# Performance work log

Hardware: AMD Instinct MI355X
Metric: run time of the kernel (lower is better)

## Reference

```python
import jax, jax.numpy as jnp
import numpy as np

S, B, H, NH = 2048, 2, 1024, 16
DH = H // NH

def setup_inputs() -> dict:
    key = jax.random.key(0)
    ks = jax.random.split(key, 4)
    x = jax.random.normal(ks[0], (S, B, H), dtype=jnp.float32)
    attention_mask = jnp.ones((B, 1, S, S), dtype=bool)
    rotary_pos_emb = jax.random.uniform(ks[1], (S, 1, 1, DH), dtype=jnp.float32)
    Wqkv = jax.random.normal(ks[2], (H, 3 * H), dtype=jnp.float32) * (1.0 / np.sqrt(H))
    bqkv = jnp.zeros((3 * H,), dtype=jnp.float32)
    Wproj = jax.random.normal(ks[3], (H, H), dtype=jnp.float32) * (1.0 / np.sqrt(H))
    bproj = jnp.zeros((H,), dtype=jnp.float32)
    return {"x": x, "attention_mask": attention_mask, "rotary_pos_emb": rotary_pos_emb,
            "Wqkv": Wqkv, "bqkv": bqkv, "Wproj": Wproj, "bproj": bproj}

def reference(x, attention_mask, rotary_pos_emb, Wqkv, bqkv, Wproj, bproj):
    s, b, h = x.shape
    dh = h // NH
    # QKV projection; per-head layout [s,b,NH,3*dh] then split (matches view+chunk)
    qkv = (x @ Wqkv + bqkv).reshape(s, b, NH, 3 * dh)
    q, k, v = jnp.split(qkv, 3, axis=-1)  # each [s,b,NH,dh]
    # RoPE (non-interleaved, rot_dim == head_dim)
    cos = jnp.cos(rotary_pos_emb)  # [s,1,1,dh]
    sin = jnp.sin(rotary_pos_emb)
    def rope(t):
        t1, t2 = jnp.split(t, 2, axis=-1)
        return t * cos + jnp.concatenate((-t2, t1), axis=-1) * sin
    q = rope(q)
    k = rope(k)
    scale = 1.0 / np.sqrt(dh).astype(np.float32)
    # scores: [b,NH,t,s]
    scores = jnp.einsum('tbhd,sbhd->bhts', q, k) * scale
    scores = jnp.where(attention_mask, scores, jnp.float32(-1e9))
    attn = jax.nn.softmax(scores, axis=-1)
    out = jnp.einsum('bhts,sbhd->tbhd', attn, v).reshape(s, b, h)
    return out @ Wproj + bproj
```

## Files before the change

kernel.cpp:

```cpp
#include <hip/hip_runtime.h>
#include <hip/hip_bf16.h>

typedef __attribute__((ext_vector_type(8))) short bf16x8;
typedef __attribute__((ext_vector_type(4))) float f32x4;
typedef __attribute__((ext_vector_type(16))) float f32x16;
typedef __attribute__((ext_vector_type(4))) unsigned short u16x4;

#define S_LEN 2048
#define BATCH 2
#define NHEAD 16
#define DHEAD 64
#define HD    1024
#define MROWS 4096
#define NQKV  3072
#define NBH   32
#define KSPLIT 2
#define KSEG  (S_LEN / KSPLIT)

static __device__ __forceinline__ unsigned short f2bf(float f) {
  union { float f; unsigned u; } v; v.f = f;
  unsigned r = v.u + 0x7FFFu + ((v.u >> 16) & 1u);
  return (unsigned short)(r >> 16);
}
static __device__ __forceinline__ float bf2f(unsigned short h) {
  union { unsigned u; float f; } v; v.u = ((unsigned)h) << 16;
  return v.f;
}
static __device__ __forceinline__ unsigned cvt_pk(float a, float b) {
  unsigned r;
  asm("v_cvt_pk_bf16_f32 %0, %1, %2" : "=v"(r) : "v"(a), "v"(b));
  return r;
}
static __device__ __forceinline__ float exp2_hw(float x) {
  float r;
  asm("v_exp_f32 %0, %1" : "=v"(r) : "v"(x));
  return r;
}

static __device__ __forceinline__ void gl_lds16(const void* g, void* l) {
  __builtin_amdgcn_global_load_lds(
      (__attribute__((address_space(1))) void*)g,
      (__attribute__((address_space(3))) void*)l, 16, 0, 0);
}

__global__ void k_cvt(const float* __restrict__ in, unsigned short* __restrict__ out, int n4) {
  int idx = blockIdx.x * blockDim.x + threadIdx.x;
  int stride = gridDim.x * blockDim.x;
  for (int i = idx; i < n4; i += stride) {
    float4 v = reinterpret_cast<const float4*>(in)[i];
    u16x4 o;
    o.x = f2bf(v.x); o.y = f2bf(v.y); o.z = f2bf(v.z); o.w = f2bf(v.w);
    reinterpret_cast<u16x4*>(out)[i] = o;
  }
}

__global__ void k_transw(const float* __restrict__ W, unsigned short* __restrict__ Wt,
                         int K, int N) {
  __shared__ unsigned short tile[64][72];
  int n0 = blockIdx.x * 64, k0 = blockIdx.y * 64;
  int t = threadIdx.x;
  int r  = t >> 2;
  int c4 = (t & 3) * 16;
  const float* src = W + (size_t)(k0 + r) * N + n0 + c4;
#pragma unroll
  for (int j = 0; j < 16; j += 4) {
    float4 v = *reinterpret_cast<const float4*>(src + j);
    tile[r][c4 + j + 0] = f2bf(v.x);
    tile[r][c4 + j + 1] = f2bf(v.y);
    tile[r][c4 + j + 2] = f2bf(v.z);
    tile[r][c4 + j + 3] = f2bf(v.w);
  }
  __syncthreads();
  int rn = t >> 2;
  int kc = (t & 3) * 16;
  unsigned short* dst = Wt + (size_t)(n0 + rn) * K + k0 + kc;
#pragma unroll
  for (int j = 0; j < 16; j += 8) {
    bf16x8 o;
#pragma unroll
    for (int e = 0; e < 8; ++e) o[e] = (short)tile[kc + j + e][rn];
    *reinterpret_cast<bf16x8*>(dst + j) = o;
  }
}

template <int OUT_BF16, int BN>
__global__ void __launch_bounds__(256)
k_gemm(const unsigned short* __restrict__ A, const unsigned short* __restrict__ Bt,
       const float* __restrict__ bias, void* __restrict__ Cout, int M, int N, int K) {
  constexpr int NF = BN / 32;
  __shared__ unsigned short As[128 * 32];
  __shared__ unsigned short Bs[BN * 32];
  int t = threadIdx.x;
  int lane = t & 63;
  int w = t >> 6;
  int g = lane >> 4, i = lane & 15;
  int wr = w >> 1, wc = w & 1;
  int bx = blockIdx.x, by = blockIdx.y;

  f32x4 acc[4][NF] = {};

  int rowS = ((t >> 6) << 4) + (t & 15);
  int colS = ((t >> 4) & 3) * 8;
  const unsigned short* a_s0 = A  + (size_t)(by * 128 + rowS) * K + colS;
  const unsigned short* a_s1 = A  + (size_t)(by * 128 + 64 + rowS) * K + colS;
  const unsigned short* b_s0 = Bt + (size_t)(bx * BN + rowS) * K + colS;
  const unsigned short* b_s1 = Bt + (size_t)(bx * BN + 64 + rowS) * K + colS;
  unsigned short* a_d0 = &As[t * 8];
  unsigned short* a_d1 = &As[(256 + t) * 8];
  unsigned short* b_d0 = &Bs[t * 8];
  unsigned short* b_d1 = &Bs[(256 + t) * 8];

  for (int kt = 0; kt < K; kt += 32) {
    __syncthreads();
    gl_lds16(a_s0 + kt, a_d0);
    gl_lds16(a_s1 + kt, a_d1);
    gl_lds16(b_s0 + kt, b_d0);
    if constexpr (BN == 128) gl_lds16(b_s1 + kt, b_d1);
    __syncthreads();

    bf16x8 af[4], bf[NF];
#pragma unroll
    for (int m = 0; m < 4; ++m)
      af[m] = *reinterpret_cast<const bf16x8*>(&As[(wr * 256 + m * 64 + lane) * 8]);
#pragma unroll
    for (int n = 0; n < NF; ++n)
      bf[n] = *reinterpret_cast<const bf16x8*>(&Bs[((wc * NF + n) * 64 + lane) * 8]);
#pragma unroll
    for (int m = 0; m < 4; ++m)
#pragma unroll
      for (int n = 0; n < NF; ++n)
        acc[m][n] = __builtin_amdgcn_mfma_f32_16x16x32_bf16(af[m], bf[n], acc[m][n], 0, 0, 0);
  }

  int crow0 = by * 128 + wr * 64;
  int ccol0 = bx * BN + wc * (BN / 2);
#pragma unroll
  for (int n = 0; n < NF; ++n) {
    int col = ccol0 + n * 16 + i;
    float bv = bias[col];
#pragma unroll
    for (int m = 0; m < 4; ++m) {
#pragma unroll
      for (int r = 0; r < 4; ++r) {
        int row = crow0 + m * 16 + g * 4 + r;
        float v = acc[m][n][r] + bv;
        if (OUT_BF16)
          reinterpret_cast<unsigned short*>(Cout)[(size_t)row * N + col] = f2bf(v);
        else
          reinterpret_cast<float*>(Cout)[(size_t)row * N + col] = v;
      }
    }
  }
}

__global__ void k_rope(const unsigned short* __restrict__ QKV, const float* __restrict__ rot,
                       unsigned short* __restrict__ Qg, unsigned short* __restrict__ Kg,
                       unsigned short* __restrict__ Vg) {
  __shared__ unsigned short vtile[32][72];
  int s0 = blockIdx.x * 32;
  int bh = blockIdx.y;
  int b = bh >> 4, nh = bh & 15;
  int t = threadIdx.x;
  int c  = t & 31;
  int hi = (t >> 5) & 1;
  int ks = t >> 6;
  int d0 = ks * 16 + hi * 8;
  int s = s0 + c;
  const unsigned short* base = QKV + ((size_t)s * BATCH + b) * NQKV + nh * 192;

  float cs[8], sn[8];
#pragma unroll
  for (int j = 0; j < 8; j += 4) {
    float4 rv = *reinterpret_cast<const float4*>(rot + (size_t)s * DHEAD + d0 + j);
    cs[j + 0] = cosf(rv.x); sn[j + 0] = sinf(rv.x);
    cs[j + 1] = cosf(rv.y); sn[j + 1] = sinf(rv.y);
    cs[j + 2] = cosf(rv.z); sn[j + 2] = sinf(rv.z);
    cs[j + 3] = cosf(rv.w); sn[j + 3] = sinf(rv.w);
  }
  float sgn = (d0 < 32) ? -1.f : 1.f;
  bf16x8 qv = *reinterpret_cast<const bf16x8*>(base + d0);
  bf16x8 qp = *reinterpret_cast<const bf16x8*>(base + (d0 ^ 32));
  bf16x8 kv = *reinterpret_cast<const bf16x8*>(base + 64 + d0);
  bf16x8 kp = *reinterpret_cast<const bf16x8*>(base + 64 + (d0 ^ 32));
  bf16x8 qo, ko;
#pragma unroll
  for (int j = 0; j < 8; ++j) {
    float q = bf2f((unsigned short)qv[j]) * cs[j] + sgn * bf2f((unsigned short)qp[j]) * sn[j];
    float k = bf2f((unsigned short)kv[j]) * cs[j] + sgn * bf2f((unsigned short)kp[j]) * sn[j];
    qo[j] = (short)f2bf(q * 0.18033688f);
    ko[j] = (short)f2bf(k);
  }
  size_t blk = ((size_t)bh * (S_LEN / 32) + (s0 >> 5)) * 2048;
  *reinterpret_cast<bf16x8*>(Qg + blk + t * 8) = qo;
  *reinterpret_cast<bf16x8*>(Kg + blk + t * 8) = ko;

  bf16x8 vv = *reinterpret_cast<const bf16x8*>(base + 128 + d0);
  *reinterpret_cast<bf16x8*>(&vtile[c][d0]) = vv;
  __syncthreads();
  int vbr = t >> 7, h = (t >> 6) & 1, hi2 = (t >> 5) & 1, cc = t & 31;
  int d = 32 * h + cc;
  bf16x8 vo;
#pragma unroll
  for (int j = 0; j < 8; ++j) vo[j] = (short)vtile[vbr * 16 + hi2 * 8 + j][d];
  size_t vblk = ((size_t)bh * (S_LEN / 16) + (s0 >> 4) + vbr) * 1024;
  *reinterpret_cast<bf16x8*>(Vg + vblk + (t & 127) * 8) = vo;
}


static __device__ __forceinline__ void sm_pv(const f32x16& sc, const bf16x8* vfr,
                                             float& l_acc, f32x16& o0, f32x16& o1) {
  float p[16];
#pragma unroll
  for (int r = 0; r < 16; ++r) p[r] = exp2_hw(sc[r]);
  float s0 = (p[0] + p[1]) + (p[2] + p[3]);
  float s1 = (p[4] + p[5]) + (p[6] + p[7]);
  float s2 = (p[8] + p[9]) + (p[10] + p[11]);
  float s3 = (p[12] + p[13]) + (p[14] + p[15]);
  l_acc += (s0 + s1) + (s2 + s3);
#pragma unroll
  for (int ksl = 0; ksl < 2; ++ksl) {
    unsigned A0 = cvt_pk(p[8 * ksl + 0], p[8 * ksl + 1]);
    unsigned A1 = cvt_pk(p[8 * ksl + 2], p[8 * ksl + 3]);
    unsigned A2 = cvt_pk(p[8 * ksl + 4], p[8 * ksl + 5]);
    unsigned A3 = cvt_pk(p[8 * ksl + 6], p[8 * ksl + 7]);
    asm volatile("v_permlane32_swap_b32 %0, %1" : "+v"(A0), "+v"(A2));
    asm volatile("v_permlane32_swap_b32 %0, %1" : "+v"(A1), "+v"(A3));
    union { unsigned u[4]; bf16x8 v; } pa;
    pa.u[0] = A0; pa.u[1] = A1; pa.u[2] = A2; pa.u[3] = A3;
    __builtin_amdgcn_s_setprio(1);
    o0 = __builtin_amdgcn_mfma_f32_32x32x16_bf16(pa.v, vfr[2 * ksl + 0], o0, 0, 0, 0);
    o1 = __builtin_amdgcn_mfma_f32_32x32x16_bf16(pa.v, vfr[2 * ksl + 1], o1, 0, 0, 0);
    __builtin_amdgcn_s_setprio(0);
  }
}

__global__ void __launch_bounds__(256, 2)
k_flash(const unsigned short* __restrict__ Qg, const unsigned short* __restrict__ Kg,
        const unsigned short* __restrict__ Vg, unsigned short* __restrict__ Opart,
        float* __restrict__ Lpart) {
  __shared__ unsigned short kv_lds[2 * 8192];
  int bh = blockIdx.x, qt = blockIdx.y, kv = blockIdx.z;
  int t = threadIdx.x, lane = t & 63;
  int c = lane & 31, hi = lane >> 5;

  int q0 = qt * 128 + (t >> 6) * 32;
  int kv0 = kv * KSEG;
  const unsigned short* Qb = Qg + (size_t)bh * S_LEN * DHEAD + (size_t)q0 * DHEAD;
  const unsigned short* Kb = Kg + (size_t)bh * S_LEN * DHEAD;
  const unsigned short* Vb = Vg + (size_t)bh * S_LEN * DHEAD;

  bf16x8 qf[4];
#pragma unroll
  for (int ks = 0; ks < 4; ++ks)
    qf[ks] = *reinterpret_cast<const bf16x8*>(Qb + ((size_t)ks * 64 + lane) * 8);

#define STAGE(kt, bufi) do {                                                   \
    const unsigned short* _ks = Kb + (size_t)(kt) * DHEAD;                     \
    const unsigned short* _vs = Vb + (size_t)(kt) * DHEAD;                     \
    unsigned short* _kd = &kv_lds[(bufi) * 8192];                              \
    unsigned short* _vd = _kd + 4096;                                          \
    gl_lds16(_ks + t * 8, _kd + t * 8);                                        \
    gl_lds16(_ks + (t + 256) * 8, _kd + (t + 256) * 8);                        \
    gl_lds16(_vs + t * 8, _vd + t * 8);                                        \
    gl_lds16(_vs + (t + 256) * 8, _vd + (t + 256) * 8);                        \
  } while (0)

  f32x16 o0 = {}, o1 = {};
  float l_acc = 0.f;
  int cur = 0;

  STAGE(kv0, 0);
  for (int kt = kv0; kt < kv0 + KSEG; kt += 64) {
    __syncthreads();
    int nxt = kv0 + (((kt - kv0) + 64) & (KSEG - 1));
    STAGE(nxt, cur ^ 1);

    const unsigned short* kbuf = &kv_lds[cur * 8192];
    const unsigned short* vbuf = kbuf + 4096;

    f32x16 scA = {}, scB = {};
    __builtin_amdgcn_s_setprio(1);
#pragma unroll
    for (int ks = 0; ks < 4; ++ks) {
      bf16x8 kf = *reinterpret_cast<const bf16x8*>(kbuf + (ks * 64 + lane) * 8);
      scA = __builtin_amdgcn_mfma_f32_32x32x16_bf16(kf, qf[ks], scA, 0, 0, 0);
    }
#pragma unroll
    for (int ks = 0; ks < 4; ++ks) {
      bf16x8 kf = *reinterpret_cast<const bf16x8*>(kbuf + (256 + ks * 64 + lane) * 8);
      scB = __builtin_amdgcn_mfma_f32_32x32x16_bf16(kf, qf[ks], scB, 0, 0, 0);
    }
    __builtin_amdgcn_s_setprio(0);

    bf16x8 va[4], vb[4];
#pragma unroll
    for (int g = 0; g < 2; ++g) {
      va[2 * g + 0] = *reinterpret_cast<const bf16x8*>(vbuf + (g * 128 + lane) * 8);
      va[2 * g + 1] = *reinterpret_cast<const bf16x8*>(vbuf + (g * 128 + 64 + lane) * 8);
      vb[2 * g + 0] = *reinterpret_cast<const bf16x8*>(vbuf + ((g + 2) * 128 + lane) * 8);
      vb[2 * g + 1] = *reinterpret_cast<const bf16x8*>(vbuf + ((g + 2) * 128 + 64 + lane) * 8);
    }

    sm_pv(scA, va, l_acc, o0, o1);
    sm_pv(scB, vb, l_acc, o0, o1);
    cur ^= 1;
  }
#undef STAGE

  float l_tot = l_acc + __shfl_xor(l_acc, 32, 64);

  unsigned short* Op = Opart + ((size_t)kv * NBH + bh) * S_LEN * DHEAD;
  if (hi == 0) Lpart[((size_t)kv * NBH + bh) * S_LEN + q0 + c] = l_tot;
#pragma unroll
  for (int r = 0; r < 16; ++r) {
    int crow = (r & 3) + 8 * (r >> 2) + 4 * hi;
    size_t rowoff = (size_t)(q0 + crow) * DHEAD;
    Op[rowoff + c]      = f2bf(o0[r]);
    Op[rowoff + 32 + c] = f2bf(o1[r]);
  }
}

__global__ void k_reduce(const unsigned short* __restrict__ Op, const float* __restrict__ Lp,
                         unsigned short* __restrict__ attn) {
  const int kvO = NBH * S_LEN * DHEAD;
  const int kvL = NBH * S_LEN;
  int idx = blockIdx.x * blockDim.x + threadIdx.x;
  int row = idx >> 3;
  int d0 = (idx & 7) * 8;
  bf16x8 a = *reinterpret_cast<const bf16x8*>(Op + (size_t)row * DHEAD + d0);
  bf16x8 bq = *reinterpret_cast<const bf16x8*>(Op + kvO + (size_t)row * DHEAD + d0);
  float inv = 1.0f / (Lp[row] + Lp[kvL + row]);
  int bh = row >> 11, q = row & (S_LEN - 1);
  int b = bh >> 4, nh = bh & 15;
  bf16x8 o;
#pragma unroll
  for (int j = 0; j < 8; ++j)
    o[j] = (short)f2bf((bf2f((unsigned short)a[j]) + bf2f((unsigned short)bq[j])) * inv);
  unsigned short* dst = attn + ((size_t)q * BATCH + b) * HD + nh * DHEAD + d0;
  *reinterpret_cast<bf16x8*>(dst) = o;
}

extern "C" void kernel_launch(void* const* d_in, const int* in_sizes, int n_in,
                              void* d_out, int out_size, void* d_ws, size_t ws_size,
                              hipStream_t stream) {
  const float* x     = (const float*)d_in[0];
  const float* rot   = (const float*)d_in[2];
  const float* Wqkv  = (const float*)d_in[3];
  const float* bqkv  = (const float*)d_in[4];
  const float* Wproj = (const float*)d_in[5];
  const float* bproj = (const float*)d_in[6];
  float* out = (float*)d_out;

  char* ws = (char*)d_ws;
  unsigned short* xb   = (unsigned short*)(ws);
  unsigned short* Wqt  = (unsigned short*)(ws + 8388608);
  unsigned short* Wpt  = (unsigned short*)(ws + 14680064);
  unsigned short* QKV  = (unsigned short*)(ws + 16777216);
  unsigned short* Qs   = (unsigned short*)(ws + 41943040);
  unsigned short* Kst  = (unsigned short*)(ws + 50331648);
  unsigned short* Vtt  = (unsigned short*)(ws + 58720256);
  unsigned short* Opart = (unsigned short*)(ws + 16777216);
  float*          Lpart = (float*)(ws + 33554432);
  unsigned short* attn  = xb;

  k_cvt<<<2048, 256, 0, stream>>>(x, xb, MROWS * HD / 4);
  k_transw<<<dim3(NQKV / 64, HD / 64), 256, 0, stream>>>(Wqkv, Wqt, HD, NQKV);
  k_transw<<<dim3(HD / 64, HD / 64), 256, 0, stream>>>(Wproj, Wpt, HD, HD);
  k_gemm<1, 128><<<dim3(NQKV / 128, MROWS / 128), 256, 0, stream>>>(xb, Wqt, bqkv, QKV,
                                                                    MROWS, NQKV, HD);
  k_rope<<<dim3(S_LEN / 32, BATCH * NHEAD), 256, 0, stream>>>(QKV, rot, Qs, Kst, Vtt);
  k_flash<<<dim3(NBH, S_LEN / 128, KSPLIT), 256, 0, stream>>>(Qs, Kst, Vtt, Opart, Lpart);
  k_reduce<<<(NBH * S_LEN * 8) / 256, 256, 0, stream>>>(Opart, Lpart, attn);
  k_gemm<0, 64><<<dim3(HD / 64, MROWS / 128), 256, 0, stream>>>(attn, Wpt, bproj, out,
                                                                MROWS, HD, HD);
}
```

Before: 158.8 us.

## Pre-tile GEMM operands into fragment-major layout for contiguous LDS loads

The producer kernels (x conversion, weight transpose, attention reduce) now write their outputs in a tile-blocked layout matching the GEMM's 64x32 LDS tile order. Each GEMM k-step then loads one fully contiguous 4KB chunk per operand tile instead of strided 16-byte row segments. Converting x and reducing attention output now go through an LDS tile to reorder, which adds shared-memory traffic and a barrier to those small kernels.

Result: faster. 134.8 us (-15.1%).

```diff
diff --git a/kernel.cpp b/kernel.cpp
--- a/kernel.cpp
+++ b/kernel.cpp
@@ -17,6 +17,7 @@
 #define KSPLIT 2
 #define KSEG  (S_LEN / KSPLIT)
 
+
 static __device__ __forceinline__ unsigned short f2bf(float f) {
   union { float f; unsigned u; } v; v.f = f;
   unsigned r = v.u + 0x7FFFu + ((v.u >> 16) & 1u);
@@ -43,15 +44,22 @@
       (__attribute__((address_space(3))) void*)l, 16, 0, 0);
 }
 
-__global__ void k_cvt(const float* __restrict__ in, unsigned short* __restrict__ out, int n4) {
-  int idx = blockIdx.x * blockDim.x + threadIdx.x;
-  int stride = gridDim.x * blockDim.x;
-  for (int i = idx; i < n4; i += stride) {
-    float4 v = reinterpret_cast<const float4*>(in)[i];
-    u16x4 o;
-    o.x = f2bf(v.x); o.y = f2bf(v.y); o.z = f2bf(v.z); o.w = f2bf(v.w);
-    reinterpret_cast<u16x4*>(out)[i] = o;
-  }
+__global__ void k_cvt(const float* __restrict__ x, unsigned short* __restrict__ Xfm) {
+  __shared__ float ltile[64][36];
+  int mt = blockIdx.x, kp = blockIdx.y;
+  int t = threadIdx.x;
+  int r = t >> 3, c4 = t & 7;
+  const float* src = x + (size_t)(mt * 64 + r) * HD + kp * 32 + c4 * 4;
+  float4 v0 = *reinterpret_cast<const float4*>(src);
+  float4 v1 = *reinterpret_cast<const float4*>(src + (size_t)32 * HD);
+  *reinterpret_cast<float4*>(&ltile[r][c4 * 4]) = v0;
+  *reinterpret_cast<float4*>(&ltile[r + 32][c4 * 4]) = v1;
+  __syncthreads();
+  int rowin = ((t >> 6) << 4) + (t & 15), ch = (t >> 4) & 3;
+  bf16x8 o;
+#pragma unroll
+  for (int e = 0; e < 8; ++e) o[e] = (short)f2bf(ltile[rowin][ch * 8 + e]);
+  *reinterpret_cast<bf16x8*>(Xfm + (((size_t)mt * 32 + kp) * 256 + t) * 8) = o;
 }
 
 __global__ void k_transw(const float* __restrict__ W, unsigned short* __restrict__ Wt,
@@ -71,15 +79,15 @@
     tile[r][c4 + j + 3] = f2bf(v.w);
   }
   __syncthreads();
-  int rn = t >> 2;
-  int kc = (t & 3) * 16;
-  unsigned short* dst = Wt + (size_t)(n0 + rn) * K + k0 + kc;
-#pragma unroll
-  for (int j = 0; j < 16; j += 8) {
+  int rowin = ((t >> 6) << 4) + (t & 15), ch = (t >> 4) & 3;
+  int nt = blockIdx.x;
+  int KP = K >> 5;
+#pragma unroll
+  for (int p = 0; p < 2; ++p) {
     bf16x8 o;
 #pragma unroll
-    for (int e = 0; e < 8; ++e) o[e] = (short)tile[kc + j + e][rn];
-    *reinterpret_cast<bf16x8*>(dst + j) = o;
+    for (int e = 0; e < 8; ++e) o[e] = (short)tile[p * 32 + ch * 8 + e][rowin];
+    *reinterpret_cast<bf16x8*>(Wt + (((size_t)nt * KP + (k0 >> 5) + p) * 256 + t) * 8) = o;
   }
 }
 
@@ -99,23 +107,23 @@
 
   f32x4 acc[4][NF] = {};
 
-  int rowS = ((t >> 6) << 4) + (t & 15);
-  int colS = ((t >> 4) & 3) * 8;
-  const unsigned short* a_s0 = A  + (size_t)(by * 128 + rowS) * K + colS;
-  const unsigned short* a_s1 = A  + (size_t)(by * 128 + 64 + rowS) * K + colS;
-  const unsigned short* b_s0 = Bt + (size_t)(bx * BN + rowS) * K + colS;
-  const unsigned short* b_s1 = Bt + (size_t)(bx * BN + 64 + rowS) * K + colS;
+  const size_t tstride = (size_t)K * 64;
+  const unsigned short* a_s0 = A  + (size_t)(2 * by) * tstride + t * 8;
+  const unsigned short* a_s1 = a_s0 + tstride;
+  const unsigned short* b_s0 = Bt + (size_t)(bx * (BN / 64)) * tstride + t * 8;
+  const unsigned short* b_s1 = b_s0 + tstride;
   unsigned short* a_d0 = &As[t * 8];
   unsigned short* a_d1 = &As[(256 + t) * 8];
   unsigned short* b_d0 = &Bs[t * 8];
   unsigned short* b_d1 = &Bs[(256 + t) * 8];
 
   for (int kt = 0; kt < K; kt += 32) {
+    size_t koff = (size_t)kt * 64;
     __syncthreads();
-    gl_lds16(a_s0 + kt, a_d0);
-    gl_lds16(a_s1 + kt, a_d1);
-    gl_lds16(b_s0 + kt, b_d0);
-    if constexpr (BN == 128) gl_lds16(b_s1 + kt, b_d1);
+    gl_lds16(a_s0 + koff, a_d0);
+    gl_lds16(a_s1 + koff, a_d1);
+    gl_lds16(b_s0 + koff, b_d0);
+    if constexpr (BN == 128) gl_lds16(b_s1 + koff, b_d1);
     __syncthreads();
 
     bf16x8 af[4], bf[NF];
@@ -206,7 +214,6 @@
   *reinterpret_cast<bf16x8*>(Vg + vblk + (t & 127) * 8) = vo;
 }
 
-
 static __device__ __forceinline__ void sm_pv(const f32x16& sc, const bf16x8* vfr,
                                              float& l_acc, f32x16& o0, f32x16& o1) {
   float p[16];
@@ -321,23 +328,42 @@
 }
 
 __global__ void k_reduce(const unsigned short* __restrict__ Op, const float* __restrict__ Lp,
-                         unsigned short* __restrict__ attn) {
+                         unsigned short* __restrict__ Afm) {
+  __shared__ unsigned short lds[64][72];
   const int kvO = NBH * S_LEN * DHEAD;
   const int kvL = NBH * S_LEN;
-  int idx = blockIdx.x * blockDim.x + threadIdx.x;
-  int row = idx >> 3;
-  int d0 = (idx & 7) * 8;
-  bf16x8 a = *reinterpret_cast<const bf16x8*>(Op + (size_t)row * DHEAD + d0);
-  bf16x8 bq = *reinterpret_cast<const bf16x8*>(Op + kvO + (size_t)row * DHEAD + d0);
-  float inv = 1.0f / (Lp[row] + Lp[kvL + row]);
-  int bh = row >> 11, q = row & (S_LEN - 1);
-  int b = bh >> 4, nh = bh & 15;
-  bf16x8 o;
-#pragma unroll
-  for (int j = 0; j < 8; ++j)
-    o[j] = (short)f2bf((bf2f((unsigned short)a[j]) + bf2f((unsigned short)bq[j])) * inv);
-  unsigned short* dst = attn + ((size_t)q * BATCH + b) * HD + nh * DHEAD + d0;
-  *reinterpret_cast<bf16x8*>(dst) = o;
+  int mt = blockIdx.x, nh = blockIdx.y;
+  int t = threadIdx.x;
+  int lq = (t >> 3) & 31, gd = t & 7;
+  int qg = mt * 32 + lq;
+
+  bf16x8 gr[4];
+#pragma unroll
+  for (int kvb = 0; kvb < 4; ++kvb) {
+    int kv = kvb >> 1, b = kvb & 1;
+    gr[kvb] = *reinterpret_cast<const bf16x8*>(
+        Op + (size_t)kv * kvO + ((size_t)(b * 16 + nh) * S_LEN + qg) * DHEAD + gd * 8);
+  }
+#pragma unroll
+  for (int b = 0; b < 2; ++b) {
+    size_t li = (size_t)(b * 16 + nh) * S_LEN + qg;
+    float inv = 1.0f / (Lp[li] + Lp[kvL + li]);
+    bf16x8 o;
+#pragma unroll
+    for (int e = 0; e < 8; ++e)
+      o[e] = (short)f2bf((bf2f((unsigned short)gr[b][e]) +
+                          bf2f((unsigned short)gr[2 + b][e])) * inv);
+    *reinterpret_cast<bf16x8*>(&lds[b * 32 + lq][gd * 8]) = o;
+  }
+  __syncthreads();
+
+  int rowin = ((t >> 6) << 4) + (t & 15), ch = (t >> 4) & 3;
+  int lr = (rowin & 1) * 32 + (rowin >> 1);
+#pragma unroll
+  for (int p = 0; p < 2; ++p) {
+    bf16x8 o = *reinterpret_cast<const bf16x8*>(&lds[lr][p * 32 + ch * 8]);
+    *reinterpret_cast<bf16x8*>(Afm + (((size_t)mt * 32 + nh * 2 + p) * 256 + t) * 8) = o;
+  }
 }
 
 extern "C" void kernel_launch(void* const* d_in, const int* in_sizes, int n_in,
@@ -363,14 +389,14 @@
   float*          Lpart = (float*)(ws + 33554432);
   unsigned short* attn  = xb;
 
-  k_cvt<<<2048, 256, 0, stream>>>(x, xb, MROWS * HD / 4);
+  k_cvt<<<dim3(MROWS / 64, HD / 32), 256, 0, stream>>>(x, xb);
   k_transw<<<dim3(NQKV / 64, HD / 64), 256, 0, stream>>>(Wqkv, Wqt, HD, NQKV);
   k_transw<<<dim3(HD / 64, HD / 64), 256, 0, stream>>>(Wproj, Wpt, HD, HD);
   k_gemm<1, 128><<<dim3(NQKV / 128, MROWS / 128), 256, 0, stream>>>(xb, Wqt, bqkv, QKV,
                                                                     MROWS, NQKV, HD);
   k_rope<<<dim3(S_LEN / 32, BATCH * NHEAD), 256, 0, stream>>>(QKV, rot, Qs, Kst, Vtt);
   k_flash<<<dim3(NBH, S_LEN / 128, KSPLIT), 256, 0, stream>>>(Qs, Kst, Vtt, Opart, Lpart);
-  k_reduce<<<(NBH * S_LEN * 8) / 256, 256, 0, stream>>>(Opart, Lpart, attn);
+  k_reduce<<<dim3(MROWS / 64, NHEAD), 256, 0, stream>>>(Opart, Lpart, attn);
   k_gemm<0, 64><<<dim3(HD / 64, MROWS / 128), 256, 0, stream>>>(attn, Wpt, bproj, out,
                                                                 MROWS, HD, HD);
 }
```
